# Kernel tuning notes

Hardware: AMD Instinct MI355X
Metric: run time of the kernel (lower is better)

## Reference

```python
import jax, jax.numpy as jnp
import numpy as np
from jax import lax

B, T, C = 4, 1024, 1024
NH, HD = 16, 64
SCALE = 1.0 / np.sqrt(HD)
LN_EPS = 1e-5


def _layernorm(x, g, b):
    mu = jnp.mean(x, axis=-1, keepdims=True)
    var = jnp.var(x, axis=-1, keepdims=True)
    return (x - mu) * lax.rsqrt(var + LN_EPS) * g + b


def _compress(seg, w, g, b):
    # seg: [B, nH, L, hd]; depthwise Conv1d(k=2, s=2, p=1, groups=hd, no bias) + LayerNorm(hd)
    Bs, nH, L, hd = seg.shape
    xc = seg.reshape(Bs * nH, L, hd).transpose(0, 2, 1)  # [B*nH, hd, L]
    y = lax.conv_general_dilated(xc, w, window_strides=(2,), padding=[(1, 1)],
                                 dimension_numbers=('NCH', 'OIH', 'NCH'),
                                 feature_group_count=hd)  # [B*nH, hd, L//2+1]
    y = y.transpose(0, 2, 1)
    y = _layernorm(y, g, b)
    return y.reshape(Bs, nH, -1, hd)


def setup_inputs() -> dict:
    key = jax.random.key(0)
    ks = jax.random.split(key, 16)
    d = {
        'x': jax.random.normal(ks[0], (B, T, C), jnp.float32),
        'mem_k1': jax.random.normal(ks[1], (B, NH, 129, HD), jnp.float32),
        'mem_v1': jax.random.normal(ks[2], (B, NH, 129, HD), jnp.float32),
        'mem_k2': jax.random.normal(ks[3], (B, NH, 257, HD), jnp.float32),
        'mem_v2': jax.random.normal(ks[4], (B, NH, 257, HD), jnp.float32),
        'mem_k3': jax.random.normal(ks[5], (B, NH, 513, HD), jnp.float32),
        'mem_v3': jax.random.normal(ks[6], (B, NH, 513, HD), jnp.float32),
        'c_attn_w': jax.random.normal(ks[7], (3 * C, C), jnp.float32) * 0.02,
        'c_attn_b': jnp.zeros((3 * C,), jnp.float32),
        'c_proj_w': jax.random.normal(ks[8], (C, C), jnp.float32) * 0.02,
        'c_proj_b': jnp.zeros((C,), jnp.float32),
        'compress_k_w': jax.random.normal(ks[9], (HD, 1, 2), jnp.float32) * 0.5,
        'ln_k_g': jnp.ones((HD,), jnp.float32),
        'ln_k_b': jnp.zeros((HD,), jnp.float32),
        'compress_v_w': jax.random.normal(ks[10], (HD, 1, 2), jnp.float32) * 0.5,
        'ln_v_g': jnp.ones((HD,), jnp.float32),
        'ln_v_b': jnp.zeros((HD,), jnp.float32),
    }
    return d


def reference(x, mem_k1, mem_v1, mem_k2, mem_v2, mem_k3, mem_v3,
              c_attn_w, c_attn_b, c_proj_w, c_proj_b,
              compress_k_w, ln_k_g, ln_k_b, compress_v_w, ln_v_g, ln_v_b):
    # qkv projection
    qkv = x @ c_attn_w.T + c_attn_b  # [B, T, 3C]
    q, k_new, v_new = jnp.split(qkv, 3, axis=2)
    q = q.reshape(B, T, NH, HD).transpose(0, 2, 1, 3)       # [B, nH, T, hd]
    k_new = k_new.reshape(B, T, NH, HD).transpose(0, 2, 1, 3)
    v_new = v_new.reshape(B, T, NH, HD).transpose(0, 2, 1, 3)

    # compress the most recent cached segment (513 -> 257)
    k3c = _compress(mem_k3, compress_k_w, ln_k_g, ln_k_b)
    v3c = _compress(mem_v3, compress_v_w, ln_v_g, ln_v_b)

    all_k = jnp.concatenate([mem_k1, mem_k2, k3c, k_new], axis=2)  # [B, nH, T_mem, hd]
    all_v = jnp.concatenate([mem_v1, mem_v2, v3c, v_new], axis=2)
    T_mem = all_k.shape[2]

    att = jnp.einsum('bhqd,bhkd->bhqk', q, all_k) * SCALE  # [B, nH, T, T_mem]
    # causal mask taken from tril(block_size)[:T, :T_mem]: row i attends cols j <= i
    mask = jnp.arange(T)[:, None] >= jnp.arange(T_mem)[None, :]
    att = jnp.where(mask, att, -jnp.inf)
    att = jax.nn.softmax(att, axis=-1)
    y = jnp.einsum('bhqk,bhkd->bhqd', att, all_v)  # [B, nH, T, hd]
    y = y.transpose(0, 2, 1, 3).reshape(B, T, C)
    y = y @ c_proj_w.T + c_proj_b
    return y
```

## Files before the change

kernel.cpp:

```cpp
#include <hip/hip_runtime.h>


using u16    = unsigned short;
using bf16x8 = __attribute__((ext_vector_type(8))) __bf16;
using f32x4  = __attribute__((ext_vector_type(4))) float;
using u16x8  = __attribute__((ext_vector_type(8))) unsigned short;
using u16x4  = __attribute__((ext_vector_type(4))) unsigned short;

__device__ __forceinline__ u16 f2bf(float f) {
    union { float f; unsigned u; } v; v.f = f;
    unsigned r = v.u + 0x7FFFu + ((v.u >> 16) & 1u);
    return (u16)(r >> 16);
}

__device__ __forceinline__ void gload16(const void* src, const void* lds_base) {
    __builtin_amdgcn_global_load_lds(
        (const __attribute__((address_space(1))) void*)src,
        (__attribute__((address_space(3))) void*)lds_base, 16, 0, 0);
}

__global__ void cvt_f32_bf16(const float* __restrict__ src, u16* __restrict__ dst, int n4) {
    int i = blockIdx.x * blockDim.x + threadIdx.x;
    if (i >= n4) return;
    float4 f = reinterpret_cast<const float4*>(src)[i];
    u16x4 o; o[0] = f2bf(f.x); o[1] = f2bf(f.y); o[2] = f2bf(f.z); o[3] = f2bf(f.w);
    reinterpret_cast<u16x4*>(dst)[i] = o;
}

__global__ __launch_bounds__(64) void copy_mem_rows(const float* __restrict__ src,
                                                    u16* __restrict__ dst, int L, int ro) {
    int bh = blockIdx.y, t = blockIdx.x, d = threadIdx.x;
    float v = src[((size_t)bh * L + t) * 64 + d];
    dst[((size_t)bh * 1024 + ro + t) * 64 + d] = f2bf(v);
}

__global__ __launch_bounds__(64) void compress_ln(const float* __restrict__ src,
                                                  const float* __restrict__ w,
                                                  const float* __restrict__ g,
                                                  const float* __restrict__ bta,
                                                  u16* __restrict__ dst, int ro) {
    int bh = blockIdx.y, t = blockIdx.x, d = threadIdx.x;
    const float* seg = src + (size_t)bh * 513 * 64;
    float x0 = (t > 0) ? seg[(size_t)(2 * t - 1) * 64 + d] : 0.f;
    float x1 = seg[(size_t)(2 * t) * 64 + d];
    float y = w[2 * d] * x0 + w[2 * d + 1] * x1;
    float s = y;
    #pragma unroll
    for (int o = 32; o; o >>= 1) s += __shfl_xor(s, o);
    float mu = s * (1.f / 64.f);
    float dv = y - mu;
    float s2 = dv * dv;
    #pragma unroll
    for (int o = 32; o; o >>= 1) s2 += __shfl_xor(s2, o);
    float var = s2 * (1.f / 64.f);
    float out = dv * rsqrtf(var + 1e-5f) * g[d] + bta[d];
    dst[((size_t)bh * 1024 + ro + t) * 64 + d] = f2bf(out);
}

__global__ __launch_bounds__(256) void transpose_v(const u16* __restrict__ src,
                                                   u16* __restrict__ dst) {
    __shared__ u16 tile[64][66];
    const int bh = blockIdx.y, t0 = blockIdx.x * 64;
    const int tid = threadIdx.x;
    #pragma unroll
    for (int i = 0; i < 2; ++i) {
        int p = tid + i * 256;
        int tr = p >> 3, dc = (p & 7) * 8;
        *(u16x8*)&tile[tr][dc] = *(const u16x8*)&src[((size_t)bh * 1024 + t0 + tr) * 64 + dc];
    }
    __syncthreads();
    #pragma unroll
    for (int i = 0; i < 2; ++i) {
        int p = tid + i * 256;
        int d = p >> 3, tc = (p & 7) * 8;
        u16x8 v;
        #pragma unroll
        for (int e = 0; e < 8; ++e) v[e] = tile[tc + e][d];
        *(u16x8*)&dst[((size_t)bh * 64 + d) * 1024 + t0 + tc] = v;
    }
}

__global__ __launch_bounds__(256) void gemm128(const u16* __restrict__ A,
                                               const u16* __restrict__ Bw,
                                               const float* __restrict__ bias,
                                               int K, int N, int mode,
                                               float* __restrict__ outF,
                                               u16* __restrict__ q_buf,
                                               u16* __restrict__ all_k,
                                               u16* __restrict__ all_v) {
    __shared__ __align__(16) u16 Al[128 * 64];
    __shared__ __align__(16) u16 Bl[128 * 64];
    const int tid = threadIdx.x;
    const int wv = tid >> 6, lane = tid & 63;
    const int lg = lane >> 4, lr = lane & 15;
    const int wr = (wv >> 1) * 64, wc = (wv & 1) * 64;
    const int m0 = blockIdx.x * 128, n0 = blockIdx.y * 128;
    f32x4 acc[4][4] = {};
    const int ob0 = wv * 4096;
    for (int kt = 0; kt < K; kt += 64) {
        __syncthreads();
        #pragma unroll
        for (int c = 0; c < 4; ++c) {
            int ob = ob0 + c * 1024;
            int o = ob + lane * 16;
            int r = o >> 7, cb = o & 127;
            gload16((const char*)A + (((size_t)(m0 + r) * K + kt) << 1) + cb, (char*)Al + ob);
            gload16((const char*)Bw + (((size_t)(n0 + r) * K + kt) << 1) + cb, (char*)Bl + ob);
        }
        __syncthreads();
        #pragma unroll
        for (int dh = 0; dh < 2; ++dh) {
            bf16x8 af[4], bq[4];
            #pragma unroll
            for (int mi = 0; mi < 4; ++mi)
                af[mi] = *(const bf16x8*)&Al[(wr + mi * 16 + lr) * 64 + dh * 32 + lg * 8];
            #pragma unroll
            for (int ni = 0; ni < 4; ++ni)
                bq[ni] = *(const bf16x8*)&Bl[(wc + ni * 16 + lr) * 64 + dh * 32 + lg * 8];
            __builtin_amdgcn_s_setprio(1);
            #pragma unroll
            for (int mi = 0; mi < 4; ++mi)
                #pragma unroll
                for (int ni = 0; ni < 4; ++ni)
                    acc[mi][ni] = __builtin_amdgcn_mfma_f32_16x16x32_bf16(af[mi], bq[ni], acc[mi][ni], 0, 0, 0);
            __builtin_amdgcn_s_setprio(0);
        }
    }
    #pragma unroll
    for (int mi = 0; mi < 4; ++mi)
        #pragma unroll
        for (int ni = 0; ni < 4; ++ni)
            #pragma unroll
            for (int r = 0; r < 4; ++r) {
                int mm = m0 + wr + mi * 16 + lg * 4 + r;
                int nn = n0 + wc + ni * 16 + lr;
                float v = acc[mi][ni][r] + bias[nn];
                if (mode == 0) {
                    outF[(size_t)mm * N + nn] = v;
                } else {
                    int which = nn >> 10, c = nn & 1023, h = c >> 6, d = c & 63;
                    int b = mm >> 10, t = mm & 1023;
                    int bh = b * 16 + h;
                    if (which == 0) {
                        q_buf[((size_t)bh * 1024 + t) * 64 + d] = f2bf(v * 0.125f);
                    } else if (t < 381) {
                        u16* dst = (which == 1) ? all_k : all_v;
                        dst[((size_t)bh * 1024 + 643 + t) * 64 + d] = f2bf(v);
                    }
                }
            }
}

__global__ __launch_bounds__(256) void attn_kernel(const u16* __restrict__ Q,
                                                   const u16* __restrict__ Kc,
                                                   const u16* __restrict__ VT,
                                                   u16* __restrict__ Y) {
    __shared__ __align__(16) u16 Kl[2][4096];
    __shared__ __align__(16) u16 Vl[2][4096];
    __shared__ __align__(16) u16 P_w[4][16 * 64];
    const int tid = threadIdx.x;
    const int lane = tid & 63;
    const int w = tid >> 6;
    const int lg = lane >> 4, lr = lane & 15;
    const int bh = blockIdx.x;
    const int pair = blockIdx.y;
    const u16* Kb = Kc + (size_t)bh * 65536;
    const u16* Vb = VT + (size_t)bh * 65536;
    char* Pbase = (char*)&P_w[w][0];
    const int xorq = (lr & 7) << 4;

    const int r0 = tid >> 3,         c0 = ((tid & 7) * 16) ^ ((r0 & 7) << 4);
    const int r1 = (tid + 256) >> 3, c1 = ((tid & 7) * 16) ^ ((r1 & 7) << 4);
    const int dst0 = w * 1024;

    for (int phase = 0; phase < 2; ++phase) {
        const int qt = phase ? (15 - pair) : pair;
        const int q0 = qt * 64;
        const u16* Qb = Q + ((size_t)bh * 1024 + q0 + w * 16) * 64;
        bf16x8 qf0 = *(const bf16x8*)&Qb[lr * 64 + lg * 8];
        bf16x8 qf1 = *(const bf16x8*)&Qb[lr * 64 + 32 + lg * 8];
        f32x4 o[4] = {};
        float m = -1e30f, lsum = 0.f;
        const int i_q = q0 + w * 16 + lr;

        {
            const char* Ks = (const char*)Kb;
            gload16(Ks + ((size_t)r0 << 7) + c0, (char*)&Kl[0][0] + dst0);
            gload16(Ks + ((size_t)r1 << 7) + c1, (char*)&Kl[0][0] + 4096 + dst0);
            gload16((const char*)Vb + ((size_t)r0 << 11) + c0, (char*)&Vl[0][0] + dst0);
            gload16((const char*)Vb + ((size_t)r1 << 11) + c1, (char*)&Vl[0][0] + 4096 + dst0);
        }
        __syncthreads();
        int cur = 0;

        for (int kt = 0; kt <= qt; ++kt) {
            if (kt < qt) {
                const int k0n = (kt + 1) * 64;
                const char* Ks = (const char*)Kb + ((size_t)k0n << 7);
                const char* Vs = (const char*)Vb + ((size_t)k0n << 1);
                char* Kd = (char*)&Kl[cur ^ 1][0];
                char* Vd = (char*)&Vl[cur ^ 1][0];
                gload16(Ks + ((size_t)r0 << 7) + c0, Kd + dst0);
                gload16(Ks + ((size_t)r1 << 7) + c1, Kd + 4096 + dst0);
                gload16(Vs + ((size_t)r0 << 11) + c0, Vd + dst0);
                gload16(Vs + ((size_t)r1 << 11) + c1, Vd + 4096 + dst0);
            }
            const char* Kt = (const char*)&Kl[cur][0];
            const char* Vt = (const char*)&Vl[cur][0];
            f32x4 st[4] = {};
            __builtin_amdgcn_s_setprio(1);
            #pragma unroll
            for (int hh = 0; hh < 4; ++hh) {
                const char* Kr = Kt + (size_t)(hh * 16 + lr) * 128;
                bf16x8 kf0 = *(const bf16x8*)(Kr + ((lg * 16) ^ xorq));
                bf16x8 kf1 = *(const bf16x8*)(Kr + ((64 + lg * 16) ^ xorq));
                st[hh] = __builtin_amdgcn_mfma_f32_16x16x32_bf16(kf0, qf0, st[hh], 0, 0, 0);
                st[hh] = __builtin_amdgcn_mfma_f32_16x16x32_bf16(kf1, qf1, st[hh], 0, 0, 0);
            }
            __builtin_amdgcn_s_setprio(0);
            const int k0 = kt * 64;
            float sv[16];
            float tmax = -1e30f;
            if (kt == qt) {
                #pragma unroll
                for (int hh = 0; hh < 4; ++hh)
                    #pragma unroll
                    for (int r = 0; r < 4; ++r) {
                        int j = k0 + hh * 16 + lg * 4 + r;
                        float s = (j <= i_q) ? st[hh][r] : -1e30f;
                        sv[hh * 4 + r] = s;
                        tmax = fmaxf(tmax, s);
                    }
            } else {
                #pragma unroll
                for (int hh = 0; hh < 4; ++hh)
                    #pragma unroll
                    for (int r = 0; r < 4; ++r) {
                        float s = st[hh][r];
                        sv[hh * 4 + r] = s;
                        tmax = fmaxf(tmax, s);
                    }
            }
            tmax = fmaxf(tmax, __shfl_xor(tmax, 16));
            tmax = fmaxf(tmax, __shfl_xor(tmax, 32));
            if (!__all(tmax - m <= 8.f)) {
                float mnew = fmaxf(m, tmax);
                float alpha = __expf(m - mnew);
                #pragma unroll
                for (int c = 0; c < 4; ++c) {
                    o[c][0] *= alpha; o[c][1] *= alpha; o[c][2] *= alpha; o[c][3] *= alpha;
                }
                lsum *= alpha;
                m = mnew;
            }
            float psum = 0.f;
            #pragma unroll
            for (int hh = 0; hh < 4; ++hh) {
                u16x4 pk;
                #pragma unroll
                for (int r = 0; r < 4; ++r) {
                    float p = __expf(sv[hh * 4 + r] - m);
                    psum += p;
                    pk[r] = f2bf(p);
                }
                *(u16x4*)(Pbase + lr * 128 + ((hh * 32 + lg * 8) ^ xorq)) = pk;
            }
            psum += __shfl_xor(psum, 16);
            psum += __shfl_xor(psum, 32);
            lsum += psum;
            asm volatile("s_waitcnt lgkmcnt(0)" ::: "memory");
            __builtin_amdgcn_sched_barrier(0);
            #pragma unroll
            for (int ks = 0; ks < 2; ++ks) {
                bf16x8 pf = *(const bf16x8*)(Pbase + lr * 128 + ((ks * 64 + lg * 16) ^ xorq));
                __builtin_amdgcn_s_setprio(1);
                #pragma unroll
                for (int c = 0; c < 4; ++c) {
                    const char* Vr = Vt + (size_t)(c * 16 + lr) * 128;
                    bf16x8 vf = *(const bf16x8*)(Vr + ((ks * 64 + lg * 16) ^ xorq));
                    o[c] = __builtin_amdgcn_mfma_f32_16x16x32_bf16(vf, pf, o[c], 0, 0, 0);
                }
                __builtin_amdgcn_s_setprio(0);
            }
            __syncthreads();
            cur ^= 1;
        }
        float inv = 1.0f / lsum;
        #pragma unroll
        for (int c = 0; c < 4; ++c) {
            u16x4 ov;
            #pragma unroll
            for (int r = 0; r < 4; ++r) ov[r] = f2bf(o[c][r] * inv);
            *(u16x4*)(Pbase + lr * 128 + (((c * 16 + lg * 4) * 2) ^ xorq)) = ov;
        }
        asm volatile("s_waitcnt lgkmcnt(0)" ::: "memory");
        __builtin_amdgcn_sched_barrier(0);
        const int b = bh >> 4, h = bh & 15;
        const int qr = lane >> 2, dseg = (lane & 3) * 16;
        const int xorr = (qr & 7) << 4;
        size_t g = ((size_t)(b * 1024 + q0 + w * 16 + qr)) * 1024 + h * 64 + dseg;
        *(u16x8*)&Y[g]     = *(const u16x8*)(Pbase + qr * 128 + ((dseg * 2) ^ xorr));
        *(u16x8*)&Y[g + 8] = *(const u16x8*)(Pbase + qr * 128 + ((dseg * 2 + 16) ^ xorr));
    }
}

extern "C" void kernel_launch(void* const* d_in, const int* in_sizes, int n_in,
                              void* d_out, int out_size, void* d_ws, size_t ws_size,
                              hipStream_t stream) {
    const float* x            = (const float*)d_in[0];
    const float* mem_k1       = (const float*)d_in[1];
    const float* mem_v1       = (const float*)d_in[2];
    const float* mem_k2       = (const float*)d_in[3];
    const float* mem_v2       = (const float*)d_in[4];
    const float* mem_k3       = (const float*)d_in[5];
    const float* mem_v3       = (const float*)d_in[6];
    const float* c_attn_w     = (const float*)d_in[7];
    const float* c_attn_b     = (const float*)d_in[8];
    const float* c_proj_w     = (const float*)d_in[9];
    const float* c_proj_b     = (const float*)d_in[10];
    const float* compress_k_w = (const float*)d_in[11];
    const float* ln_k_g       = (const float*)d_in[12];
    const float* ln_k_b       = (const float*)d_in[13];
    const float* compress_v_w = (const float*)d_in[14];
    const float* ln_v_g       = (const float*)d_in[15];
    const float* ln_v_b       = (const float*)d_in[16];

    char* ws = (char*)d_ws;
    u16* x_bf   = (u16*)(ws);
    u16* all_vT = (u16*)(ws);
    u16* wq_bf  = (u16*)(ws + (8u << 20));
    u16* wp_bf  = (u16*)(ws + (14u << 20));
    u16* q_buf  = (u16*)(ws + (16u << 20));
    u16* all_k  = (u16*)(ws + (24u << 20));
    u16* all_v  = (u16*)(ws + (32u << 20));
    u16* att_y  = (u16*)(ws + (40u << 20));
    float* out = (float*)d_out;

    cvt_f32_bf16<<<4096, 256, 0, stream>>>(x, x_bf, 1048576);
    cvt_f32_bf16<<<3072, 256, 0, stream>>>(c_attn_w, wq_bf, 786432);
    cvt_f32_bf16<<<1024, 256, 0, stream>>>(c_proj_w, wp_bf, 262144);

    copy_mem_rows<<<dim3(129, 64), 64, 0, stream>>>(mem_k1, all_k, 129, 0);
    copy_mem_rows<<<dim3(129, 64), 64, 0, stream>>>(mem_v1, all_v, 129, 0);
    copy_mem_rows<<<dim3(257, 64), 64, 0, stream>>>(mem_k2, all_k, 257, 129);
    copy_mem_rows<<<dim3(257, 64), 64, 0, stream>>>(mem_v2, all_v, 257, 129);

    compress_ln<<<dim3(257, 64), 64, 0, stream>>>(mem_k3, compress_k_w, ln_k_g, ln_k_b, all_k, 386);
    compress_ln<<<dim3(257, 64), 64, 0, stream>>>(mem_v3, compress_v_w, ln_v_g, ln_v_b, all_v, 386);

    gemm128<<<dim3(32, 24), 256, 0, stream>>>(x_bf, wq_bf, c_attn_b, 1024, 3072, 1,
                                              nullptr, q_buf, all_k, all_v);

    transpose_v<<<dim3(16, 64), 256, 0, stream>>>(all_v, all_vT);

    attn_kernel<<<dim3(64, 8), 256, 0, stream>>>(q_buf, all_k, all_vT, att_y);

    gemm128<<<dim3(32, 8), 256, 0, stream>>>(att_y, wp_bf, c_proj_b, 1024, 1024, 0,
                                             out, nullptr, nullptr, nullptr);
}
```

Measured before the change: 140.4 us.

## Replace LDS-staged GEMM with direct global-to-register double-buffered MFMA GEMM

Rewrites the projection GEMM so each wave loads its MFMA operands straight from global memory into registers, double-buffered across K steps, instead of staging tiles through LDS with barriers. It also adds an XCD-aware block index remap and uses smaller 64x64 tiles for the output projection to launch more blocks. This removes LDS traffic and syncs, but loses the data reuse LDS gave across waves, so global and L2 traffic goes up. The K loop is hard-coded to 32 steps (K=1024).

New measurement: 227.1 us. 1.62x slower.

```diff
diff --git a/kernel.cpp b/kernel.cpp
--- a/kernel.cpp
+++ b/kernel.cpp
@@ -80,62 +80,71 @@
     }
 }
 
-__global__ __launch_bounds__(256) void gemm128(const u16* __restrict__ A,
-                                               const u16* __restrict__ Bw,
-                                               const float* __restrict__ bias,
-                                               int K, int N, int mode,
-                                               float* __restrict__ outF,
-                                               u16* __restrict__ q_buf,
-                                               u16* __restrict__ all_k,
-                                               u16* __restrict__ all_v) {
-    __shared__ __align__(16) u16 Al[128 * 64];
-    __shared__ __align__(16) u16 Bl[128 * 64];
+template<int MI, int NI, int MODE>
+__global__ __launch_bounds__(256) void gemm_direct(const u16* __restrict__ A,
+                                                   const u16* __restrict__ Bw,
+                                                   const float* __restrict__ bias,
+                                                   int K, int N,
+                                                   float* __restrict__ outF,
+                                                   u16* __restrict__ q_buf,
+                                                   u16* __restrict__ all_k,
+                                                   u16* __restrict__ all_v) {
+    constexpr int BM = MI * 32, BN = NI * 32;
     const int tid = threadIdx.x;
     const int wv = tid >> 6, lane = tid & 63;
     const int lg = lane >> 4, lr = lane & 15;
-    const int wr = (wv >> 1) * 64, wc = (wv & 1) * 64;
-    const int m0 = blockIdx.x * 128, n0 = blockIdx.y * 128;
-    f32x4 acc[4][4] = {};
-    const int ob0 = wv * 4096;
-    for (int kt = 0; kt < K; kt += 64) {
-        __syncthreads();
+    const int wr = (wv >> 1) * (MI * 16), wc = (wv & 1) * (NI * 16);
+    const int id = blockIdx.x + blockIdx.y * gridDim.x;
+    const int per = (gridDim.x * gridDim.y) >> 3;
+    const int nid = (id & 7) * per + (id >> 3);
+    const int m0 = (nid % gridDim.x) * BM;
+    const int n0 = (nid / gridDim.x) * BN;
+
+    const char* pA[MI];
+    const char* pB[NI];
+    #pragma unroll
+    for (int mi = 0; mi < MI; ++mi)
+        pA[mi] = (const char*)(A + (size_t)(m0 + wr + mi * 16 + lr) * K + lg * 8);
+    #pragma unroll
+    for (int ni = 0; ni < NI; ++ni)
+        pB[ni] = (const char*)(Bw + (size_t)(n0 + wc + ni * 16 + lr) * K + lg * 8);
+
+    f32x4 acc[MI][NI] = {};
+    bf16x8 a0[MI], a1[MI], b0[NI], b1[NI];
+    #pragma unroll
+    for (int mi = 0; mi < MI; ++mi) a0[mi] = *(const bf16x8*)(pA[mi]);
+    #pragma unroll
+    for (int ni = 0; ni < NI; ++ni) b0[ni] = *(const bf16x8*)(pB[ni]);
+
+    #pragma unroll
+    for (int kt = 0; kt < 32; ++kt) {
+        if (kt + 1 < 32) {
+            bf16x8* an = (kt & 1) ? a0 : a1;
+            bf16x8* bn = (kt & 1) ? b0 : b1;
+            #pragma unroll
+            for (int mi = 0; mi < MI; ++mi) an[mi] = *(const bf16x8*)(pA[mi] + (kt + 1) * 64);
+            #pragma unroll
+            for (int ni = 0; ni < NI; ++ni) bn[ni] = *(const bf16x8*)(pB[ni] + (kt + 1) * 64);
+        }
+        const bf16x8* ac = (kt & 1) ? a1 : a0;
+        const bf16x8* bc = (kt & 1) ? b1 : b0;
         #pragma unroll
-        for (int c = 0; c < 4; ++c) {
-            int ob = ob0 + c * 1024;
-            int o = ob + lane * 16;
-            int r = o >> 7, cb = o & 127;
-            gload16((const char*)A + (((size_t)(m0 + r) * K + kt) << 1) + cb, (char*)Al + ob);
-            gload16((const char*)Bw + (((size_t)(n0 + r) * K + kt) << 1) + cb, (char*)Bl + ob);
-        }
-        __syncthreads();
+        for (int mi = 0; mi < MI; ++mi)
+            #pragma unroll
+            for (int ni = 0; ni < NI; ++ni)
+                acc[mi][ni] = __builtin_amdgcn_mfma_f32_16x16x32_bf16(ac[mi], bc[ni], acc[mi][ni], 0, 0, 0);
+    }
+
+    #pragma unroll
+    for (int mi = 0; mi < MI; ++mi)
         #pragma unroll
-        for (int dh = 0; dh < 2; ++dh) {
-            bf16x8 af[4], bq[4];
-            #pragma unroll
-            for (int mi = 0; mi < 4; ++mi)
-                af[mi] = *(const bf16x8*)&Al[(wr + mi * 16 + lr) * 64 + dh * 32 + lg * 8];
-            #pragma unroll
-            for (int ni = 0; ni < 4; ++ni)
-                bq[ni] = *(const bf16x8*)&Bl[(wc + ni * 16 + lr) * 64 + dh * 32 + lg * 8];
-            __builtin_amdgcn_s_setprio(1);
-            #pragma unroll
-            for (int mi = 0; mi < 4; ++mi)
-                #pragma unroll
-                for (int ni = 0; ni < 4; ++ni)
-                    acc[mi][ni] = __builtin_amdgcn_mfma_f32_16x16x32_bf16(af[mi], bq[ni], acc[mi][ni], 0, 0, 0);
-            __builtin_amdgcn_s_setprio(0);
-        }
-    }
-    #pragma unroll
-    for (int mi = 0; mi < 4; ++mi)
-        #pragma unroll
-        for (int ni = 0; ni < 4; ++ni)
+        for (int ni = 0; ni < NI; ++ni)
             #pragma unroll
             for (int r = 0; r < 4; ++r) {
                 int mm = m0 + wr + mi * 16 + lg * 4 + r;
                 int nn = n0 + wc + ni * 16 + lr;
                 float v = acc[mi][ni][r] + bias[nn];
-                if (mode == 0) {
+                if (MODE == 0) {
                     outF[(size_t)mm * N + nn] = v;
                 } else {
                     int which = nn >> 10, c = nn & 1023, h = c >> 6, d = c & 63;
@@ -348,13 +357,13 @@
     compress_ln<<<dim3(257, 64), 64, 0, stream>>>(mem_k3, compress_k_w, ln_k_g, ln_k_b, all_k, 386);
     compress_ln<<<dim3(257, 64), 64, 0, stream>>>(mem_v3, compress_v_w, ln_v_g, ln_v_b, all_v, 386);
 
-    gemm128<<<dim3(32, 24), 256, 0, stream>>>(x_bf, wq_bf, c_attn_b, 1024, 3072, 1,
-                                              nullptr, q_buf, all_k, all_v);
+    gemm_direct<4, 4, 1><<<dim3(32, 24), 256, 0, stream>>>(
+        x_bf, wq_bf, c_attn_b, 1024, 3072, nullptr, q_buf, all_k, all_v);
 
     transpose_v<<<dim3(16, 64), 256, 0, stream>>>(all_v, all_vT);
 
     attn_kernel<<<dim3(64, 8), 256, 0, stream>>>(q_buf, all_k, all_vT, att_y);
 
-    gemm128<<<dim3(32, 8), 256, 0, stream>>>(att_y, wp_bf, c_proj_b, 1024, 1024, 0,
-                                             out, nullptr, nullptr, nullptr);
-}
+    gemm_direct<2, 2, 0><<<dim3(64, 16), 256, 0, stream>>>(
+        att_y, wp_bf, c_proj_b, 1024, 1024, out, nullptr, nullptr, nullptr);
+}
```
